# Optimization experiments

Measured on AMD Instinct MI355X. Metric: run time of the kernel, lower is better.

## Reference

```python
import jax, jax.numpy as jnp
import numpy as np
import math

B, T, C = 4, 2048, 1024
H, D = 16, 64            # num_heads, head_dim
ORIG_LEN = 4096
MIN_FREQ, MAX_FREQ = 0.5, 40.0


def setup_inputs() -> dict:
    key = jax.random.key(0)
    ks = jax.random.split(key, 6)
    x = jax.random.normal(ks[0], (B, T, C), dtype=jnp.float32)
    keep_idx = jnp.sort(jax.random.randint(ks[1], (B, T, 1), 0, ORIG_LEN), axis=1)
    W_qkv = jax.random.normal(ks[2], (C, 3 * C), dtype=jnp.float32) * (1.0 / math.sqrt(C))
    b_qkv = jnp.zeros((3 * C,), dtype=jnp.float32)
    W_proj = jax.random.normal(ks[3], (C, C), dtype=jnp.float32) * (1.0 / math.sqrt(C))
    b_proj = jnp.zeros((C,), dtype=jnp.float32)
    return {"x": x, "keep_idx": keep_idx, "original_seq_len": ORIG_LEN,
            "W_qkv": W_qkv, "b_qkv": b_qkv, "W_proj": W_proj, "b_proj": b_proj}


def _rope_angles(positions, orig_len):
    # positions: [b, t] float token positions in the ORIGINAL sequence.
    # golden_gate 1-D RoPE: normalized positions times geometric frequency band.
    half = D // 2
    freqs = MIN_FREQ * (MAX_FREQ / MIN_FREQ) ** (jnp.arange(half, dtype=jnp.float32) / (half - 1))
    pos_norm = positions / jnp.float32(orig_len)          # [b, t]
    return 2.0 * jnp.pi * pos_norm[:, :, None] * freqs    # [b, t, half]


def _apply_rope(x, cos, sin):
    # x: [b, h, t, d]; cos/sin: [b, 1, t, d/2]; rotate (first half, second half) pairs
    half = D // 2
    x1, x2 = x[..., :half], x[..., half:]
    return jnp.concatenate([x1 * cos - x2 * sin, x1 * sin + x2 * cos], axis=-1)


def reference(x, keep_idx, original_seq_len, W_qkv, b_qkv, W_proj, b_proj):
    b, t, c = x.shape
    # fused QKV projection + head split: (b,t,3c) -> (b,t,3,h,d) -> (b,h,t,3,d)
    qkv = (x @ W_qkv + b_qkv).reshape(b, t, 3, H, D).transpose(0, 3, 1, 2, 4)
    q, k, v = qkv[:, :, :, 0], qkv[:, :, :, 1], qkv[:, :, :, 2]  # each [b,h,t,d]

    positions = keep_idx[..., 0].astype(jnp.float32)             # [b, t]
    ang = _rope_angles(positions, original_seq_len)              # [b, t, d/2]
    cos = jnp.cos(ang)[:, None]                                  # [b,1,t,d/2]
    sin = jnp.sin(ang)[:, None]
    q = _apply_rope(q, cos, sin)
    k = _apply_rope(k, cos, sin)

    # dense non-causal scaled dot-product attention
    scale = 1.0 / math.sqrt(D)
    scores = jnp.einsum('bhqd,bhkd->bhqk', q, k) * scale
    attn = jax.nn.softmax(scores, axis=-1)
    out = jnp.einsum('bhqk,bhkd->bhqd', attn, v)                 # [b,h,t,d]

    out = out.transpose(0, 2, 1, 3).reshape(b, t, H * D)         # [b,t,c]
    return out @ W_proj + b_proj
```

## Files before the change

### kernel.cpp

```cpp
#include <hip/hip_runtime.h>
#include <hip/hip_bf16.h>
#include <math.h>

#define B_ 4
#define T_ 2048
#define C_ 1024
#define H_ 16
#define D_ 64

typedef __attribute__((ext_vector_type(8))) short bf16x8_t;
typedef __attribute__((ext_vector_type(4))) float f32x4_t;
typedef __attribute__((ext_vector_type(2))) unsigned int uiv2_t;

#define SHIFT2 32.0f

#define GLOAD_LDS16(gp, lp)                                                          \
    __builtin_amdgcn_global_load_lds(                                                \
        (const __attribute__((address_space(1))) void*)(gp),                         \
        (__attribute__((address_space(3))) void*)(lp), 16, 0, 0)

#define WAVE_ORDER() __builtin_amdgcn_wave_barrier()

__device__ inline short bf16bits(float f) {
    __hip_bfloat16 h = __float2bfloat16(f);
    return *reinterpret_cast<short*>(&h);
}

__device__ inline unsigned int pack2bf(float a, float b) {
    __hip_bfloat162 h = __float22bfloat162_rn(make_float2(a, b));
    return *reinterpret_cast<unsigned int*>(&h);
}

__global__ void xconv_kernel(const float* __restrict__ in,
                             __hip_bfloat16* __restrict__ out, int n4) {
    int i = blockIdx.x * blockDim.x + threadIdx.x;
    if (i < n4) {
        float4 v = *(const float4*)(in + (size_t)i * 4);
        uint2 u;
        u.x = pack2bf(v.x, v.y);
        u.y = pack2bf(v.z, v.w);
        *(uint2*)(out + (size_t)i * 4) = u;
    }
}

__global__ void rope_tab_kernel(const int* __restrict__ keep,
                                const int* __restrict__ orig,
                                float* __restrict__ tab) {
    int i = blockIdx.x * blockDim.x + threadIdx.x;
    int tok = i >> 5, d = i & 31;
    float freq = 0.5f * exp2f((float)d * (6.321928094887362f / 31.0f));
    float ang  = 6.283185307179586f * ((float)keep[tok] / (float)(*orig)) * freq;
    tab[(size_t)tok * 64 + d]      = cosf(ang);
    tab[(size_t)tok * 64 + 32 + d] = sinf(ang);
}

__global__ void transpose_conv_kernel(const float* __restrict__ in,
                                      __hip_bfloat16* __restrict__ out,
                                      int K, int N) {
    __shared__ float s[32][33];
    const int n0 = blockIdx.x * 32;
    const int k0 = blockIdx.y * 32;
    const int tx = threadIdx.x;
    const int ty = threadIdx.y;
#pragma unroll
    for (int yy = 0; yy < 32; yy += 8)
        s[ty + yy][tx] = in[(size_t)(k0 + ty + yy) * N + n0 + tx];
    __syncthreads();
#pragma unroll
    for (int yy = 0; yy < 32; yy += 8)
        out[(size_t)(n0 + ty + yy) * K + k0 + tx] = __float2bfloat16(s[tx][ty + yy]);
}

template <int MODE>
__global__ __launch_bounds__(256)
void gemm_kernel(const __hip_bfloat16* __restrict__ A,
                 const __hip_bfloat16* __restrict__ BT,
                 const float* __restrict__ bias,
                 float* __restrict__ out,
                 __hip_bfloat16* __restrict__ qbuf,
                 __hip_bfloat16* __restrict__ kbuf,
                 __hip_bfloat16* __restrict__ vtbuf,
                 const float* __restrict__ ropetab,
                 int M, int N, int K) {
    __shared__ __align__(16) __hip_bfloat16 As[128 * 32];
    __shared__ __align__(16) __hip_bfloat16 Bs[128 * 32];

    const int tid  = threadIdx.x;
    const int lane = tid & 63;
    const int wave = tid >> 6;
    const int wm   = wave >> 1;
    const int wn   = wave & 1;
    const int l15  = lane & 15;
    const int quad = lane >> 4;

    const int nT  = N >> 7;
    const int grp = blockIdx.x / (8 * nT);
    const int rem = blockIdx.x - grp * 8 * nT;
    const int m0  = (grp * 8 + (rem & 7)) * 128;
    const int n0  = (rem >> 3) * 128;

    f32x4_t acc[4][4];
#pragma unroll
    for (int i = 0; i < 4; i++)
#pragma unroll
        for (int j = 0; j < 4; j++) acc[i][j] = (f32x4_t)0.0f;

    const int lrow = lane >> 2;
    const int lcol = (lane & 3) * 8;
    const __hip_bfloat16* gA  = A  + (size_t)(m0 + wave * 16 + lrow) * K + lcol;
    const __hip_bfloat16* gA2 = gA + (size_t)64 * K;
    const __hip_bfloat16* gB  = BT + (size_t)(n0 + wave * 16 + lrow) * K + lcol;
    const __hip_bfloat16* gB2 = gB + (size_t)64 * K;
    __hip_bfloat16* lA  = As + wave * 16 * 32;
    __hip_bfloat16* lA2 = As + (64 + wave * 16) * 32;
    __hip_bfloat16* lB  = Bs + wave * 16 * 32;
    __hip_bfloat16* lB2 = Bs + (64 + wave * 16) * 32;

    for (int k0 = 0; k0 < K; k0 += 32) {
        __syncthreads();
        GLOAD_LDS16(gA  + k0, lA);
        GLOAD_LDS16(gA2 + k0, lA2);
        GLOAD_LDS16(gB  + k0, lB);
        GLOAD_LDS16(gB2 + k0, lB2);
        __syncthreads();

        bf16x8_t af[4], bfv[4];
#pragma unroll
        for (int i = 0; i < 4; i++)
            af[i] = *(const bf16x8_t*)(As + (wm * 64 + i * 16 + l15) * 32 + quad * 8);
#pragma unroll
        for (int j = 0; j < 4; j++)
            bfv[j] = *(const bf16x8_t*)(Bs + (wn * 64 + j * 16 + l15) * 32 + quad * 8);
#pragma unroll
        for (int i = 0; i < 4; i++)
#pragma unroll
            for (int j = 0; j < 4; j++)
                acc[i][j] = __builtin_amdgcn_mfma_f32_16x16x32_bf16(af[i], bfv[j], acc[i][j], 0, 0, 0);
    }

    float bv[4];
#pragma unroll
    for (int j = 0; j < 4; j++)
        bv[j] = bias[n0 + wn * 64 + j * 16 + l15];

    if (MODE == 0) {
#pragma unroll
        for (int i = 0; i < 4; i++)
#pragma unroll
            for (int r = 0; r < 4; r++) {
                int row = m0 + wm * 64 + i * 16 + quad * 4 + r;
#pragma unroll
                for (int j = 0; j < 4; j++) {
                    int col = n0 + wn * 64 + j * 16 + l15;
                    out[(size_t)row * N + col] = acc[i][j][r] + bv[j];
                }
            }
    } else {
        const int cb   = n0 + wn * 64;
        const int part = cb >> 10;
        const int h    = (cb & 1023) >> 6;
        if (part == 2) {
#pragma unroll
            for (int j = 0; j < 4; j++) {
#pragma unroll
                for (int i = 0; i < 4; i++) {
#pragma unroll
                    for (int r = 0; r < 4; r++) {
                        int row = m0 + wm * 64 + i * 16 + quad * 4 + r;
                        int b = row >> 11;
                        int t = row & 2047;
                        int d = j * 16 + l15;
                        vtbuf[((size_t)((b * H_ + h) * D_ + d)) * T_ + t] =
                            __float2bfloat16(acc[i][j][r] + bv[j]);
                    }
                }
            }
        } else {
            __hip_bfloat16* dst = (part == 0) ? qbuf : kbuf;
            const float sc = (part == 0) ? 0.18033688011112042f : 1.0f;
#pragma unroll
            for (int i = 0; i < 4; i++) {
#pragma unroll
                for (int r = 0; r < 4; r++) {
                    int row = m0 + wm * 64 + i * 16 + quad * 4 + r;
                    int b = row >> 11;
                    int t = row & 2047;
                    const float* trow = ropetab + (size_t)row * 64;
                    size_t base = ((size_t)(b * H_ + h) * T_ + t) * D_;
#pragma unroll
                    for (int j = 0; j < 2; j++) {
                        int d = j * 16 + l15;
                        float cs = trow[d];
                        float sn = trow[32 + d];
                        float x1 = acc[i][j][r]     + bv[j];
                        float x2 = acc[i][j + 2][r] + bv[j + 2];
                        dst[base + d]      = __float2bfloat16(sc * (x1 * cs - x2 * sn));
                        dst[base + d + 32] = __float2bfloat16(sc * (x1 * sn + x2 * cs));
                    }
                }
            }
        }
    }
}

#define KVTILE (64 * 64)

__global__ __launch_bounds__(256, 4)
void attn_kernel(const __hip_bfloat16* __restrict__ q,
                 const __hip_bfloat16* __restrict__ k,
                 const __hip_bfloat16* __restrict__ vt,
                 __hip_bfloat16* __restrict__ attn_out) {
    __shared__ __align__(16) __hip_bfloat16 SMEM[4 * KVTILE];

    const int tid  = threadIdx.x;
    const int lane = tid & 63;
    const int wave = tid >> 6;
    const int l15  = lane & 15;
    const int quad = lane >> 4;
    const int x7   = l15 & 7;

    const int bh = blockIdx.x & 63;
    const int qt = blockIdx.x >> 6;
    const int b  = bh >> 4;
    const int h  = bh & 15;

    const size_t qkbase = (size_t)bh * T_ * D_;
    const size_t vbase  = (size_t)bh * D_ * T_;
    const int    qrow0  = qt * 128 + wave * 32;

    const int drow   = lane >> 3;
    const int gchunk = (lane & 7) ^ drow;

    const __hip_bfloat16* kg = k + qkbase;
    const __hip_bfloat16* vg = vt + vbase;

    const int c0 = ((quad)     ^ x7) * 8;
    const int c1 = ((4 + quad) ^ x7) * 8;

    bf16x8_t qa[2][2];
#pragma unroll
    for (int qf = 0; qf < 2; qf++)
#pragma unroll
        for (int kk = 0; kk < 2; kk++)
            qa[qf][kk] = *(const bf16x8_t*)(q + qkbase +
                          (size_t)(qrow0 + qf * 16 + l15) * D_ + kk * 32 + quad * 8);

    bf16x8_t ones;
#pragma unroll
    for (int i = 0; i < 8; i++) ones[i] = (short)0x3F80;

    f32x4_t o[2][4];
#pragma unroll
    for (int qf = 0; qf < 2; qf++)
#pragma unroll
        for (int jd = 0; jd < 4; jd++) o[qf][jd] = (f32x4_t)0.0f;
    f32x4_t osum[2];
    osum[0] = (f32x4_t)0.0f;
    osum[1] = (f32x4_t)0.0f;

#pragma unroll
    for (int i = 0; i < 2; i++) {
        int r = wave * 16 + i * 8;
        GLOAD_LDS16(kg + (size_t)(r + drow) * D_ + gchunk * 8, SMEM + r * 64);
        GLOAD_LDS16(vg + (size_t)(r + drow) * T_ + gchunk * 8, SMEM + 2 * KVTILE + r * 64);
    }
    __syncthreads();

    for (int kt = 0; kt < T_ / 64; kt++) {
        const int curoff = (kt & 1) * KVTILE;
        const int nxtoff = curoff ^ KVTILE;
        if (kt + 1 < T_ / 64) {
#pragma unroll
            for (int i = 0; i < 2; i++) {
                int r = wave * 16 + i * 8;
                GLOAD_LDS16(kg + (size_t)((kt + 1) * 64 + r + drow) * D_ + gchunk * 8,
                            SMEM + nxtoff + r * 64);
                GLOAD_LDS16(vg + (size_t)(r + drow) * T_ + (kt + 1) * 64 + gchunk * 8,
                            SMEM + 2 * KVTILE + nxtoff + r * 64);
            }
        }

        const __hip_bfloat16* KLc = SMEM + curoff;
        const __hip_bfloat16* VLc = SMEM + 2 * KVTILE + curoff;

        bf16x8_t kf[4][2];
#pragma unroll
        for (int jt = 0; jt < 4; jt++) {
            kf[jt][0] = *(const bf16x8_t*)(KLc + (jt * 16 + l15) * 64 + c0);
            kf[jt][1] = *(const bf16x8_t*)(KLc + (jt * 16 + l15) * 64 + c1);
        }

        f32x4_t sT[2][4];
#pragma unroll
        for (int qf = 0; qf < 2; qf++)
#pragma unroll
            for (int jt = 0; jt < 4; jt++) sT[qf][jt] = (f32x4_t)0.0f;
#pragma unroll
        for (int jt = 0; jt < 4; jt++)
#pragma unroll
            for (int kk = 0; kk < 2; kk++)
#pragma unroll
                for (int qf = 0; qf < 2; qf++)
                    sT[qf][jt] = __builtin_amdgcn_mfma_f32_16x16x32_bf16(
                        kf[jt][kk], qa[qf][kk], sT[qf][jt], 0, 0, 0);

        bf16x8_t pb[2][2];
#pragma unroll
        for (int qf = 0; qf < 2; qf++) {
            unsigned int w0[4], w1[4];
#pragma unroll
            for (int jt = 0; jt < 4; jt++) {
                float p0 = __builtin_amdgcn_exp2f(sT[qf][jt][0] - SHIFT2);
                float p1 = __builtin_amdgcn_exp2f(sT[qf][jt][1] - SHIFT2);
                float p2 = __builtin_amdgcn_exp2f(sT[qf][jt][2] - SHIFT2);
                float p3 = __builtin_amdgcn_exp2f(sT[qf][jt][3] - SHIFT2);
                w0[jt] = pack2bf(p0, p1);
                w1[jt] = pack2bf(p2, p3);
            }
#pragma unroll
            for (int kk = 0; kk < 2; kk++) {
                uiv2_t s0 = __builtin_amdgcn_permlane32_swap(w0[2 * kk], w0[2 * kk + 1], false, false);
                uiv2_t r0 = __builtin_amdgcn_permlane16_swap(s0[0], s0[1], false, false);
                uiv2_t s1 = __builtin_amdgcn_permlane32_swap(w1[2 * kk], w1[2 * kk + 1], false, false);
                uiv2_t r1 = __builtin_amdgcn_permlane16_swap(s1[0], s1[1], false, false);
                union { unsigned int u[4]; bf16x8_t v; } pu;
                pu.u[0] = r0[0];
                pu.u[1] = r1[0];
                pu.u[2] = r0[1];
                pu.u[3] = r1[1];
                pb[qf][kk] = pu.v;
            }
        }

#pragma unroll
        for (int qf = 0; qf < 2; qf++) {
            osum[qf] = __builtin_amdgcn_mfma_f32_16x16x32_bf16(ones, pb[qf][0], osum[qf], 0, 0, 0);
            osum[qf] = __builtin_amdgcn_mfma_f32_16x16x32_bf16(ones, pb[qf][1], osum[qf], 0, 0, 0);
        }

#pragma unroll
        for (int jd = 0; jd < 4; jd++) {
            bf16x8_t vf0 = *(const bf16x8_t*)(VLc + (jd * 16 + l15) * 64 + c0);
            bf16x8_t vf1 = *(const bf16x8_t*)(VLc + (jd * 16 + l15) * 64 + c1);
#pragma unroll
            for (int qf = 0; qf < 2; qf++) {
                o[qf][jd] = __builtin_amdgcn_mfma_f32_16x16x32_bf16(vf0, pb[qf][0], o[qf][jd], 0, 0, 0);
                o[qf][jd] = __builtin_amdgcn_mfma_f32_16x16x32_bf16(vf1, pb[qf][1], o[qf][jd], 0, 0, 0);
            }
        }

        __syncthreads();
    }

    float inv[2];
    inv[0] = 1.0f / osum[0][0];
    inv[1] = 1.0f / osum[1][0];

    __hip_bfloat16* Pep = SMEM + wave * (32 * 72);

    WAVE_ORDER();
#pragma unroll
    for (int qf = 0; qf < 2; qf++) {
#pragma unroll
        for (int jd = 0; jd < 4; jd++) {
            uint2 pk;
            pk.x = pack2bf(o[qf][jd][0] * inv[qf], o[qf][jd][1] * inv[qf]);
            pk.y = pack2bf(o[qf][jd][2] * inv[qf], o[qf][jd][3] * inv[qf]);
            *(uint2*)(Pep + (qf * 16 + l15) * 72 + jd * 16 + quad * 4) = pk;
        }
    }
    WAVE_ORDER();

#pragma unroll
    for (int rnd = 0; rnd < 4; rnd++) {
        int row = rnd * 8 + (lane >> 3);
        int col = (lane & 7) * 8;
        bf16x8_t vrow = *(const bf16x8_t*)(Pep + row * 72 + col);
        int token = qt * 128 + wave * 32 + row;
        *(bf16x8_t*)(attn_out + ((size_t)(b * T_ + token)) * C_ + h * 64 + col) = vrow;
    }
}

extern "C" void kernel_launch(void* const* d_in, const int* in_sizes, int n_in,
                              void* d_out, int out_size, void* d_ws, size_t ws_size,
                              hipStream_t stream) {
    const float* x        = (const float*)d_in[0];
    const int*   keep_idx = (const int*)d_in[1];
    const int*   orig_len = (const int*)d_in[2];
    const float* Wqkv     = (const float*)d_in[3];
    const float* bqkv     = (const float*)d_in[4];
    const float* Wproj    = (const float*)d_in[5];
    const float* bproj    = (const float*)d_in[6];
    float*       out      = (float*)d_out;

    const size_t NTOK = (size_t)B_ * T_;
    const size_t QKV1 = NTOK * C_;

    __hip_bfloat16* qbuf    = (__hip_bfloat16*)d_ws;
    __hip_bfloat16* kbuf    = qbuf    + QKV1;
    __hip_bfloat16* vtbuf   = kbuf    + QKV1;
    __hip_bfloat16* attnbuf = vtbuf   + QKV1;
    __hip_bfloat16* WqkvT   = attnbuf + QKV1;
    __hip_bfloat16* WprojT  = WqkvT   + (size_t)C_ * 3 * C_;
    __hip_bfloat16* xbf     = WprojT  + (size_t)C_ * C_;
    float*          ropetab = (float*)(xbf + QKV1);

    xconv_kernel<<<(QKV1 / 4 + 255) / 256, 256, 0, stream>>>(x, xbf, (int)(QKV1 / 4));
    rope_tab_kernel<<<(NTOK * 32) / 256, 256, 0, stream>>>(keep_idx, orig_len, ropetab);

    dim3 tb(32, 8);
    transpose_conv_kernel<<<dim3(3 * C_ / 32, C_ / 32), tb, 0, stream>>>(Wqkv, WqkvT, C_, 3 * C_);
    transpose_conv_kernel<<<dim3(C_ / 32, C_ / 32), tb, 0, stream>>>(Wproj, WprojT, C_, C_);

    gemm_kernel<1><<<(8192 / 128) * (3072 / 128), 256, 0, stream>>>(
        xbf, WqkvT, bqkv, nullptr, qbuf, kbuf, vtbuf, ropetab, 8192, 3072, 1024);

    attn_kernel<<<(T_ / 128) * 64, 256, 0, stream>>>(qbuf, kbuf, vtbuf, attnbuf);

    gemm_kernel<0><<<(8192 / 128) * (1024 / 128), 256, 0, stream>>>(
        attnbuf, WprojT, bproj, out, nullptr, nullptr, nullptr, nullptr, 8192, 1024, 1024);
}
```

Measured before the change: 303.2 us.

## Double-buffer GEMM LDS tiles and use partial vmcnt waits in attention

The GEMM main loop now uses two LDS buffers per operand, so the next K-tile is issued as global-to-LDS loads while MFMAs run on the current tile. It waits only for the older loads with a partial vmcnt wait instead of a full __syncthreads. The attention kernel's existing double buffer gets the same treatment: a partial vmcnt wait plus a raw barrier, so the prefetch of the next K/V tile stays in flight. This doubles GEMM LDS use, which may lower occupancy, and it relies on hand-counted vmcnt values being correct.

```diff
diff --git a/kernel.cpp b/kernel.cpp
--- a/kernel.cpp
+++ b/kernel.cpp
@@ -70,6 +70,8 @@
     for (int yy = 0; yy < 32; yy += 8)
         out[(size_t)(n0 + ty + yy) * K + k0 + tx] = __float2bfloat16(s[tx][ty + yy]);
 }
+
+#define GTILE (128 * 32)
 
 template <int MODE>
 __global__ __launch_bounds__(256)
@@ -82,8 +84,8 @@
                  __hip_bfloat16* __restrict__ vtbuf,
                  const float* __restrict__ ropetab,
                  int M, int N, int K) {
-    __shared__ __align__(16) __hip_bfloat16 As[128 * 32];
-    __shared__ __align__(16) __hip_bfloat16 Bs[128 * 32];
+    __shared__ __align__(16) __hip_bfloat16 As[2 * GTILE];
+    __shared__ __align__(16) __hip_bfloat16 Bs[2 * GTILE];
 
     const int tid  = threadIdx.x;
     const int lane = tid & 63;
@@ -111,31 +113,46 @@
     const __hip_bfloat16* gA2 = gA + (size_t)64 * K;
     const __hip_bfloat16* gB  = BT + (size_t)(n0 + wave * 16 + lrow) * K + lcol;
     const __hip_bfloat16* gB2 = gB + (size_t)64 * K;
-    __hip_bfloat16* lA  = As + wave * 16 * 32;
-    __hip_bfloat16* lA2 = As + (64 + wave * 16) * 32;
-    __hip_bfloat16* lB  = Bs + wave * 16 * 32;
-    __hip_bfloat16* lB2 = Bs + (64 + wave * 16) * 32;
-
-    for (int k0 = 0; k0 < K; k0 += 32) {
-        __syncthreads();
-        GLOAD_LDS16(gA  + k0, lA);
-        GLOAD_LDS16(gA2 + k0, lA2);
-        GLOAD_LDS16(gB  + k0, lB);
-        GLOAD_LDS16(gB2 + k0, lB2);
-        __syncthreads();
+    const int ldsW = wave * 16 * 32;
+
+    GLOAD_LDS16(gA,  As + ldsW);
+    GLOAD_LDS16(gA2, As + ldsW + 64 * 32);
+    GLOAD_LDS16(gB,  Bs + ldsW);
+    GLOAD_LDS16(gB2, Bs + ldsW + 64 * 32);
+
+    const int NK = K >> 5;
+    for (int t = 0; t < NK; ++t) {
+        const int off = (t & 1) * GTILE;
+        if (t + 1 < NK) {
+            const int noff = off ^ GTILE;
+            const int kk   = (t + 1) << 5;
+            GLOAD_LDS16(gA  + kk, As + noff + ldsW);
+            GLOAD_LDS16(gA2 + kk, As + noff + ldsW + 64 * 32);
+            GLOAD_LDS16(gB  + kk, Bs + noff + ldsW);
+            GLOAD_LDS16(gB2 + kk, Bs + noff + ldsW + 64 * 32);
+            asm volatile("s_waitcnt vmcnt(4)" ::: "memory");
+        } else {
+            asm volatile("s_waitcnt vmcnt(0)" ::: "memory");
+        }
+        __builtin_amdgcn_s_barrier();
+        __builtin_amdgcn_sched_barrier(0);
 
         bf16x8_t af[4], bfv[4];
 #pragma unroll
         for (int i = 0; i < 4; i++)
-            af[i] = *(const bf16x8_t*)(As + (wm * 64 + i * 16 + l15) * 32 + quad * 8);
+            af[i] = *(const bf16x8_t*)(As + off + (wm * 64 + i * 16 + l15) * 32 + quad * 8);
 #pragma unroll
         for (int j = 0; j < 4; j++)
-            bfv[j] = *(const bf16x8_t*)(Bs + (wn * 64 + j * 16 + l15) * 32 + quad * 8);
+            bfv[j] = *(const bf16x8_t*)(Bs + off + (wn * 64 + j * 16 + l15) * 32 + quad * 8);
 #pragma unroll
         for (int i = 0; i < 4; i++)
 #pragma unroll
             for (int j = 0; j < 4; j++)
                 acc[i][j] = __builtin_amdgcn_mfma_f32_16x16x32_bf16(af[i], bfv[j], acc[i][j], 0, 0, 0);
+
+        __builtin_amdgcn_sched_barrier(0);
+        asm volatile("s_waitcnt lgkmcnt(0)" ::: "memory");
+        __builtin_amdgcn_s_barrier();
     }
 
     float bv[4];
@@ -264,7 +281,6 @@
         GLOAD_LDS16(kg + (size_t)(r + drow) * D_ + gchunk * 8, SMEM + r * 64);
         GLOAD_LDS16(vg + (size_t)(r + drow) * T_ + gchunk * 8, SMEM + 2 * KVTILE + r * 64);
     }
-    __syncthreads();
 
     for (int kt = 0; kt < T_ / 64; kt++) {
         const int curoff = (kt & 1) * KVTILE;
@@ -278,7 +294,12 @@
                 GLOAD_LDS16(vg + (size_t)(r + drow) * T_ + (kt + 1) * 64 + gchunk * 8,
                             SMEM + 2 * KVTILE + nxtoff + r * 64);
             }
-        }
+            asm volatile("s_waitcnt vmcnt(4)" ::: "memory");
+        } else {
+            asm volatile("s_waitcnt vmcnt(0)" ::: "memory");
+        }
+        __builtin_amdgcn_s_barrier();
+        __builtin_amdgcn_sched_barrier(0);
 
         const __hip_bfloat16* KLc = SMEM + curoff;
         const __hip_bfloat16* VLc = SMEM + 2 * KVTILE + curoff;
@@ -349,7 +370,9 @@
             }
         }
 
-        __syncthreads();
+        __builtin_amdgcn_sched_barrier(0);
+        asm volatile("s_waitcnt lgkmcnt(0)" ::: "memory");
+        __builtin_amdgcn_s_barrier();
     }
 
     float inv[2];
```

Measured after the change: 293.3 us. 1.03x faster.
